# Optimization experiments

Measured on AMD Instinct MI355X. Metric: run time of the kernel, lower is better.

The kernel has to match this reference:

```python
import jax, jax.numpy as jnp
import numpy as np

NUM_CLASSES = 1000
NUM_NODES = 1111  # 1000 leaves + 100 + 10 + 1 root
BATCH = 32768


def _build_hierarchy():
    """Deterministic 10-ary 3-level hierarchy standing in for heirachy_graph.p.

    Returns:
      A: [NUM_NODES, NUM_CLASSES] float32, A[n, l] = 1 if node n lies on leaf l's
         path to root (including leaf l itself). probs = outputs @ A.T reproduces
         the per-sample dict accumulation probs[node] += val.
      W: [NUM_CLASSES, NUM_NODES] float32 path-weight vectors:
         W[t, path[j]] += 2^-(j+1) for path root->t, plus the extra
         W[t, t] += 2^-len(path) term from the source.
    """
    parent = {}
    for l in range(1000):
        parent[l] = 1000 + l // 10
    for k in range(100):
        parent[1000 + k] = 1100 + k // 10
    for m in range(10):
        parent[1100 + m] = 1110
    parent[1110] = None

    A = np.zeros((NUM_NODES, NUM_CLASSES), dtype=np.float32)
    for l in range(NUM_CLASSES):
        node = l
        A[node, l] = 1.0
        while parent[node] is not None:
            node = parent[node]
            A[node, l] += 1.0

    W = np.zeros((NUM_CLASSES, NUM_NODES), dtype=np.float32)
    for t in range(NUM_CLASSES):
        path = [t]
        node = t
        while parent[node] is not None:
            node = parent[node]
            path = [node] + path
        for j, p in enumerate(path):
            W[t, p] += 2.0 ** (-(j + 1))
        W[t, t] += 2.0 ** (-len(path))  # extra target term in the source
    return A, W


def setup_inputs() -> dict:
    key = jax.random.key(0)
    k1, k2 = jax.random.split(key)
    outputs = jax.random.normal(k1, (BATCH, NUM_CLASSES), dtype=jnp.float32)
    target = jax.random.randint(k2, (BATCH,), 0, NUM_CLASSES, dtype=jnp.int64)
    A_np, W_np = _build_hierarchy()
    return {
        "outputs": outputs,
        "target": target,
        "A": jnp.asarray(A_np),
        "W": jnp.asarray(W_np),
    }


def reference(outputs, target, A, W):
    # probs[b, n] = sum over leaves l under node n of outputs[b, l]
    probs = outputs @ A.T                      # [B, NUM_NODES]
    w = W[target]                               # [B, NUM_NODES] gather per target
    win = jnp.einsum("bn,bn->b", probs, w)     # [B]
    return jnp.sum(1.0 - win)                  # scalar loss
```

## Files before the change

### kernel.cpp

```cpp
#include <hip/hip_runtime.h>


constexpr int BATCH   = 32768;
constexpr int NCLS    = 1000;
constexpr int BLOCKS  = 2048;
constexpr int THREADS = 256;

__device__ __forceinline__ float wchunk(const float4 v, int cc,
                                        int t0, int t1, int t2, int t3,
                                        int a0, int a1, int a2, int a3,
                                        int b0, int b1, int b2, int b3) {
    const bool hi = cc >= 500;
    const bool q1 = cc >= 250;
    const bool q3 = cc >= 750;
    const int  t  = hi ? (q3 ? t3 : t2) : (q1 ? t1 : t0);
    const int  a  = hi ? (q3 ? a3 : a2) : (q1 ? a1 : a0);
    const int  b  = hi ? (q3 ? b3 : b2) : (q1 ? b1 : b0);
    const int  r250 = hi ? (q3 ? 750 : 500) : (q1 ? 250 : 0);
    const int  l0 = (cc - r250) * 4;
    const float xs[4] = {v.x, v.y, v.z, v.w};
    float acc = 0.0f;
    #pragma unroll
    for (int j = 0; j < 4; ++j) {
        const int l = l0 + j;
        float w = 0.5f;
        if ((unsigned)(l - a) < 100u) w += 0.25f;
        if ((unsigned)(l - b) < 10u)  w += 0.125f;
        if (l == t)                   w += 0.125f;
        acc = fmaf(xs[j], w, acc);
    }
    return acc;
}

__global__ __launch_bounds__(THREADS) void hloss_part(
    const float* __restrict__ outputs,
    const int*   __restrict__ target,
    float* __restrict__ partials)
{
    __shared__ float red[4];
    const int lane = threadIdx.x & 63;
    const int wid  = threadIdx.x >> 6;
    const int rowbase = blockIdx.x * 16 + wid * 4;

    int tmine = 0;
    if (lane < 4) tmine = target[rowbase + lane];
    const int t0 = __shfl(tmine, 0, 64);
    const int t1 = __shfl(tmine, 1, 64);
    const int t2 = __shfl(tmine, 2, 64);
    const int t3 = __shfl(tmine, 3, 64);
    const int a0 = (t0 / 100) * 100, b0 = (t0 / 10) * 10;
    const int a1 = (t1 / 100) * 100, b1 = (t1 / 10) * 10;
    const int a2 = (t2 / 100) * 100, b2 = (t2 / 10) * 10;
    const int a3 = (t3 / 100) * 100, b3 = (t3 / 10) * 10;

    const float4* f4 = reinterpret_cast<const float4*>(
        outputs + (size_t)rowbase * NCLS);
    const float4 zero4 = {0.f, 0.f, 0.f, 0.f};
    float s0 = 0.f, s1 = 0.f, s2 = 0.f, s3 = 0.f;

    for (int c = lane; c < 256; c += 64) {
        const int c1 = c + 256, c2 = c + 512, c3 = c + 768;
        const float4 v0 = f4[c];
        const float4 v1 = f4[c1];
        const float4 v2 = f4[c2];
        const float4 v3 = (c3 < 1000) ? f4[c3] : zero4;
        s0 += wchunk(v0, c,  t0,t1,t2,t3, a0,a1,a2,a3, b0,b1,b2,b3);
        s1 += wchunk(v1, c1, t0,t1,t2,t3, a0,a1,a2,a3, b0,b1,b2,b3);
        s2 += wchunk(v2, c2, t0,t1,t2,t3, a0,a1,a2,a3, b0,b1,b2,b3);
        s3 += wchunk(v3, c3, t0,t1,t2,t3, a0,a1,a2,a3, b0,b1,b2,b3);
    }
    float win = (s0 + s1) + (s2 + s3);

    #pragma unroll
    for (int off = 32; off > 0; off >>= 1)
        win += __shfl_xor(win, off, 64);
    if (lane == 0) red[wid] = win;
    __syncthreads();
    if (threadIdx.x == 0)
        partials[blockIdx.x] = (red[0] + red[1]) + (red[2] + red[3]);
}

__global__ __launch_bounds__(THREADS) void hloss_final(
    const float* __restrict__ partials,
    float* __restrict__ out)
{
    __shared__ float red[4];
    const int lane = threadIdx.x & 63;
    const int wid  = threadIdx.x >> 6;
    float s = 0.0f;
    for (int i = threadIdx.x; i < BLOCKS; i += THREADS)
        s += partials[i];
    #pragma unroll
    for (int off = 32; off > 0; off >>= 1)
        s += __shfl_xor(s, off, 64);
    if (lane == 0) red[wid] = s;
    __syncthreads();
    if (threadIdx.x == 0)
        out[0] = (float)BATCH - ((red[0] + red[1]) + (red[2] + red[3]));
}

extern "C" void kernel_launch(void* const* d_in, const int* in_sizes, int n_in,
                              void* d_out, int out_size, void* d_ws, size_t ws_size,
                              hipStream_t stream) {
    const float* outputs = (const float*)d_in[0];
    const int*   target  = (const int*)d_in[1];
    float* out      = (float*)d_out;
    float* partials = (float*)d_ws;

    hloss_part <<<dim3(BLOCKS), dim3(THREADS), 0, stream>>>(outputs, target, partials);
    hloss_final<<<dim3(1),      dim3(THREADS), 0, stream>>>(partials, out);
}
```

Before: 28.83 us.

## Fuse final reduction into main kernel via last-block atomic counter

Replaces the two-kernel partial/final reduction with a single kernel in which the last block to finish (found through an atomic counter and thread fences) sums the partials and writes the loss. Block size doubles to 512 threads with half as many blocks. This removes the second kernel launch and its serialization gap, but adds a memset on the stream each call plus an atomic and fences per block.

```diff
diff --git a/kernel.cpp b/kernel.cpp
--- a/kernel.cpp
+++ b/kernel.cpp
@@ -3,8 +3,9 @@
 
 constexpr int BATCH   = 32768;
 constexpr int NCLS    = 1000;
-constexpr int BLOCKS  = 2048;
-constexpr int THREADS = 256;
+constexpr int BLOCKS  = 1024;
+constexpr int THREADS = 512;
+constexpr int WAVES   = THREADS / 64;
 
 __device__ __forceinline__ float wchunk(const float4 v, int cc,
                                         int t0, int t1, int t2, int t3,
@@ -32,15 +33,18 @@
     return acc;
 }
 
-__global__ __launch_bounds__(THREADS) void hloss_part(
+__global__ __launch_bounds__(THREADS) void hloss(
     const float* __restrict__ outputs,
     const int*   __restrict__ target,
-    float* __restrict__ partials)
+    float*       __restrict__ partials,
+    unsigned*    __restrict__ counter,
+    float*       __restrict__ out)
 {
-    __shared__ float red[4];
+    __shared__ float red[WAVES];
+    __shared__ int   lastflag;
     const int lane = threadIdx.x & 63;
     const int wid  = threadIdx.x >> 6;
-    const int rowbase = blockIdx.x * 16 + wid * 4;
+    const int rowbase = blockIdx.x * (4 * WAVES) + wid * 4;
 
     int tmine = 0;
     if (lane < 4) tmine = target[rowbase + lane];
@@ -76,27 +80,39 @@
         win += __shfl_xor(win, off, 64);
     if (lane == 0) red[wid] = win;
     __syncthreads();
-    if (threadIdx.x == 0)
-        partials[blockIdx.x] = (red[0] + red[1]) + (red[2] + red[3]);
-}
 
-__global__ __launch_bounds__(THREADS) void hloss_final(
-    const float* __restrict__ partials,
-    float* __restrict__ out)
-{
-    __shared__ float red[4];
-    const int lane = threadIdx.x & 63;
-    const int wid  = threadIdx.x >> 6;
-    float s = 0.0f;
-    for (int i = threadIdx.x; i < BLOCKS; i += THREADS)
-        s += partials[i];
-    #pragma unroll
-    for (int off = 32; off > 0; off >>= 1)
-        s += __shfl_xor(s, off, 64);
-    if (lane == 0) red[wid] = s;
+    if (threadIdx.x == 0) {
+        float p = 0.0f;
+        #pragma unroll
+        for (int i = 0; i < WAVES; ++i) p += red[i];
+        partials[blockIdx.x] = p;
+        __threadfence();
+        const unsigned old = atomicAdd(counter, 1u);
+        if (old == BLOCKS - 1) {
+            __threadfence();
+            lastflag = 1;
+        } else {
+            lastflag = 0;
+        }
+    }
     __syncthreads();
-    if (threadIdx.x == 0)
-        out[0] = (float)BATCH - ((red[0] + red[1]) + (red[2] + red[3]));
+
+    if (lastflag) {
+        float s = 0.0f;
+        for (int i = threadIdx.x; i < BLOCKS; i += THREADS)
+            s += partials[i];
+        #pragma unroll
+        for (int off = 32; off > 0; off >>= 1)
+            s += __shfl_xor(s, off, 64);
+        if (lane == 0) red[wid] = s;
+        __syncthreads();
+        if (threadIdx.x == 0) {
+            float tot = 0.0f;
+            #pragma unroll
+            for (int i = 0; i < WAVES; ++i) tot += red[i];
+            out[0] = (float)BATCH - tot;
+        }
+    }
 }
 
 extern "C" void kernel_launch(void* const* d_in, const int* in_sizes, int n_in,
@@ -104,9 +120,12 @@
                               hipStream_t stream) {
     const float* outputs = (const float*)d_in[0];
     const int*   target  = (const int*)d_in[1];
-    float* out      = (float*)d_out;
-    float* partials = (float*)d_ws;
+    float*    out      = (float*)d_out;
+    unsigned* counter  = (unsigned*)d_ws;
+    float*    partials = (float*)((char*)d_ws + 1024);
 
-    hloss_part <<<dim3(BLOCKS), dim3(THREADS), 0, stream>>>(outputs, target, partials);
-    hloss_final<<<dim3(1),      dim3(THREADS), 0, stream>>>(partials, out);
+    hipMemsetAsync(d_ws, 0, 64, stream);
+
+    hloss<<<dim3(BLOCKS), dim3(THREADS), 0, stream>>>(
+        outputs, target, partials, counter, out);
 }
```

Result: slower. 62.12 us (+115.4%).
